# Optimization experiments

Hardware: AMD Instinct MI355X
Metric: run time of the kernel (lower is better)

Reference implementation:

```python
import jax, jax.numpy as jnp
import numpy as np

N_NODES = 50000
N_EDGES = 800000
IN_CH, HID_CH, OUT_CH = 256, 128, 64


def setup_inputs() -> dict:
    key = jax.random.key(0)
    k1, k2, k3, k4 = jax.random.split(key, 4)
    x = jax.random.normal(k1, (N_NODES, IN_CH), dtype=jnp.float32)
    edge_index = jax.random.randint(k2, (2, N_EDGES), 0, N_NODES, dtype=jnp.int64)
    # Glorot-style init for the GCN weight matrices, zero bias (PyG default)
    W1 = jax.random.normal(k3, (IN_CH, HID_CH), dtype=jnp.float32) * (1.0 / np.sqrt(IN_CH))
    b1 = jnp.zeros((HID_CH,), dtype=jnp.float32)
    W2 = jax.random.normal(k4, (HID_CH, OUT_CH), dtype=jnp.float32) * (1.0 / np.sqrt(HID_CH))
    b2 = jnp.zeros((OUT_CH,), dtype=jnp.float32)
    return {"x": x, "edge_index": edge_index, "W1": W1, "b1": b1, "W2": W2, "b2": b2}


def _gcn_conv(x, W, b, src, dst, dinv_sqrt, n_nodes):
    # linear transform then degree-normalized scatter-add aggregation
    h = x @ W                                        # [N, F_out]
    norm = dinv_sqrt[src] * dinv_sqrt[dst]           # [E+N]
    msg = h[src] * norm[:, None]                     # gather + scale
    out = jax.ops.segment_sum(msg, dst, num_segments=n_nodes)
    return out + b


def reference(x, edge_index, W1, b1, W2, b2):
    n_nodes = x.shape[0]
    loops = jnp.arange(n_nodes, dtype=edge_index.dtype)
    src = jnp.concatenate([edge_index[0], loops])    # add self-loops (PyG default)
    dst = jnp.concatenate([edge_index[1], loops])
    # symmetric normalization: deg computed over targets incl. self-loops
    deg = jax.ops.segment_sum(jnp.ones_like(dst, dtype=x.dtype), dst, num_segments=n_nodes)
    dinv_sqrt = jnp.where(deg > 0, jax.lax.rsqrt(deg), 0.0)
    h = jax.nn.relu(_gcn_conv(x, W1, b1, src, dst, dinv_sqrt, n_nodes))
    return _gcn_conv(h, W2, b2, src, dst, dinv_sqrt, n_nodes)
```

## Files before the change

### kernel.cpp

```cpp
#include <hip/hip_runtime.h>


typedef __attribute__((ext_vector_type(4))) float floatx4;
typedef _Float16 __attribute__((ext_vector_type(8))) half8v;

#define BUCK_SH 6
#define BUCK    64
#define NBLK    256

#define AS1(p) ((const __attribute__((address_space(1))) void*)(p))
#define AS3(p) ((__attribute__((address_space(3))) void*)(p))

__device__ __forceinline__ int edge_id(const int* __restrict__ ei, int is64, long long pos) {
    return is64 ? ei[2 * pos] : ei[(int)pos];
}

__device__ __forceinline__ int detect_is64(const int* __restrict__ ei) {
    __shared__ int nz;
    if (threadIdx.x == 0) nz = 0;
    __syncthreads();
    if (threadIdx.x < 256 && ei[2 * threadIdx.x + 1] != 0) atomicOr(&nz, 1);
    __syncthreads();
    return (nz == 0) ? 1 : 0;
}

__device__ __forceinline__ void convW_one(const float* W, _Float16* Wt, int K, int Nc, int idx) {
    if (idx >= K * Nc) return;
    int k = idx / Nc, n = idx % Nc;
    Wt[(long long)n * K + k] = (_Float16)W[idx];
}

__global__ void __launch_bounds__(256)
hist2convW_kernel(const int* __restrict__ ei, int* __restrict__ hist2,
                  int E, int NB, int chunk,
                  const float* __restrict__ W1, _Float16* __restrict__ W1t,
                  const float* __restrict__ W2, _Float16* __restrict__ W2t) {
    __shared__ int h[1024];
    const int t = threadIdx.x;
    const int is64 = detect_is64(ei);
    for (int i = t; i < NB; i += 256) h[i] = 0;
    __syncthreads();
    const int lo = blockIdx.x * chunk;
    const int hi = min(E, lo + chunk);
    for (int e = lo + t; e < hi; e += 256) {
        int d = edge_id(ei, is64, (long long)E + e);
        atomicAdd(&h[d >> BUCK_SH], 1);
    }
    __syncthreads();
    for (int i = t; i < NB; i += 256) hist2[(long long)blockIdx.x * NB + i] = h[i];
    {
        int gtid = blockIdx.x * 256 + t;
        convW_one(W1, W1t, 256, 128, gtid);
        int g2 = gtid - 256 * 128;
        if (g2 >= 0) convW_one(W2, W2t, 128, 64, g2);
    }
}

__global__ void __launch_bounds__(256)
wavescan_kernel(const int* __restrict__ hist2, int* __restrict__ start2t,
                int* __restrict__ colsum, int NB) {
    const int wid  = (blockIdx.x * 256 + threadIdx.x) >> 6;
    const int lane = threadIdx.x & 63;
    if (wid >= NB) return;
    int carry = 0;
    for (int c = 0; c < NBLK; c += 64) {
        int v = hist2[(long long)(c + lane) * NB + wid];
        int incl = v;
#pragma unroll
        for (int s = 1; s < 64; s <<= 1) {
            int u = __shfl_up(incl, s, 64);
            if (lane >= s) incl += u;
        }
        start2t[(long long)wid * NBLK + c + lane] = carry + incl - v;
        carry += __shfl(incl, 63, 64);
    }
    if (lane == 0) colsum[wid] = carry;
}

__global__ void __launch_bounds__(1024)
basescan_kernel(const int* __restrict__ colsum, int* __restrict__ bbase, int NB, int E) {
    __shared__ int sm[1024];
    const int t = threadIdx.x;
    int v = (t < NB) ? colsum[t] : 0;
    sm[t] = v;
    __syncthreads();
    for (int s = 1; s < 1024; s <<= 1) {
        int u = (t >= s) ? sm[t - s] : 0;
        __syncthreads();
        sm[t] += u;
        __syncthreads();
    }
    if (t < NB) bbase[t] = sm[t] - v;
    if (t == 0) bbase[NB] = E;
}

__global__ void __launch_bounds__(256)
scatter2_kernel(const int* __restrict__ ei, const int* __restrict__ bbase,
                const int* __restrict__ start2t, unsigned* __restrict__ ebuf,
                int E, int NB, int chunk) {
    __shared__ int hcur[1024];
    const int t = threadIdx.x;
    const int is64 = detect_is64(ei);
    for (int i = t; i < NB; i += 256)
        hcur[i] = bbase[i] + start2t[(long long)i * NBLK + blockIdx.x];
    __syncthreads();
    const int lo = blockIdx.x * chunk;
    const int hi = min(E, lo + chunk);
    for (int e = lo + t; e < hi; e += 256) {
        int s = edge_id(ei, is64, e);
        int d = edge_id(ei, is64, (long long)E + e);
        int pos = atomicAdd(&hcur[d >> BUCK_SH], 1);
        ebuf[pos] = (unsigned)s | ((unsigned)(d & (BUCK - 1)) << 26);
    }
}

__global__ void __launch_bounds__(256)
csrbuild_kernel(const unsigned* __restrict__ ebuf, const int* __restrict__ bbase,
                int* __restrict__ offs, float* __restrict__ dinv,
                int* __restrict__ csr, int N, int NB, int E) {
    __shared__ int cnt[BUCK], exc[BUCK], cur[BUCK];
    const int b = blockIdx.x;
    const int t = threadIdx.x;
    if (t < BUCK) { cnt[t] = 0; cur[t] = 0; }
    __syncthreads();
    const int lo = bbase[b], hi = bbase[b + 1];
    for (int i = lo + t; i < hi; i += blockDim.x)
        atomicAdd(&cnt[ebuf[i] >> 26], 1);
    __syncthreads();
    if (t == 0) {
        int run = 0;
        for (int l = 0; l < BUCK; ++l) { exc[l] = run; run += cnt[l]; }
    }
    __syncthreads();
    if (t < BUCK) {
        int n = b * BUCK + t;
        if (n < N) {
            offs[n] = lo + exc[t];
            dinv[n] = rsqrtf(1.0f + (float)cnt[t]);
        }
    }
    if (b == NB - 1 && t == 0) offs[N] = E;
    for (int i = lo + t; i < hi; i += blockDim.x) {
        unsigned e = ebuf[i];
        int l = e >> 26;
        int p = lo + exc[l] + atomicAdd(&cur[l], 1);
        csr[p] = (int)(e & 0x03FFFFFFu);
    }
}

template <int NCOL, int K>
__launch_bounds__(256)
__global__ void gemm_f16_kernel(const float* __restrict__ A,
                                const _Float16* __restrict__ Bt,
                                _Float16* __restrict__ C, int M) {
    constexpr int NCB = NCOL / 16;
    constexpr int BM = 128, BK = 64;
    constexpr int NC = K / BK;
    constexpr int UNITS = BM * BK / 4;
    __shared__ float As[2][BM * BK];

    const int tid  = threadIdx.x;
    const int wave = tid >> 6;
    const int lane = tid & 63;
    const int n15  = lane & 15;
    const int q    = lane >> 4;
    const int row0 = blockIdx.x * BM;

    floatx4 acc[2][NCB];
#pragma unroll
    for (int rt = 0; rt < 2; ++rt)
#pragma unroll
        for (int c = 0; c < NCB; ++c) acc[rt][c] = (floatx4){0.f, 0.f, 0.f, 0.f};

    auto stage = [&](int buf, int kc) {
#pragma unroll
        for (int j = 0; j < UNITS / 256; ++j) {
            int g = j * 256 + tid;
            int r = g >> 4;
            int u = (g & 15) ^ (r & 15);
            int gr = row0 + r;
            if (gr >= M) gr = M - 1;
            const float* gp = &A[(long long)gr * K + kc + u * 4];
            float* lp = &As[buf][g * 4];
            __builtin_amdgcn_global_load_lds(AS1(gp), AS3(lp), 16, 0, 0);
        }
    };

    stage(0, 0);
    __syncthreads();

#pragma unroll
    for (int c = 0; c < NC; ++c) {
        if (c + 1 < NC) stage((c + 1) & 1, (c + 1) * BK);
        const int buf = c & 1;
#pragma unroll
        for (int ks = 0; ks < 2; ++ks) {
            half8v af[2];
#pragma unroll
            for (int rt = 0; rt < 2; ++rt) {
                const int R = wave * 32 + rt * 16 + n15;
                const int u0 = ks * 8 + q * 2;
                const int p0 = (u0)     ^ (R & 15);
                const int p1 = (u0 + 1) ^ (R & 15);
                float4 f0 = *(const float4*)&As[buf][R * BK + p0 * 4];
                float4 f1 = *(const float4*)&As[buf][R * BK + p1 * 4];
                af[rt][0] = (_Float16)f0.x; af[rt][1] = (_Float16)f0.y;
                af[rt][2] = (_Float16)f0.z; af[rt][3] = (_Float16)f0.w;
                af[rt][4] = (_Float16)f1.x; af[rt][5] = (_Float16)f1.y;
                af[rt][6] = (_Float16)f1.z; af[rt][7] = (_Float16)f1.w;
            }
#pragma unroll
            for (int cb = 0; cb < NCB; ++cb) {
                const _Float16* bp = &Bt[(long long)(cb * 16 + n15) * K + c * BK + ks * 32 + q * 8];
                half8v bf = *(const half8v*)bp;
                acc[0][cb] = __builtin_amdgcn_mfma_f32_16x16x32_f16(af[0], bf, acc[0][cb], 0, 0, 0);
                acc[1][cb] = __builtin_amdgcn_mfma_f32_16x16x32_f16(af[1], bf, acc[1][cb], 0, 0, 0);
            }
        }
        if (c + 1 < NC) __syncthreads();
    }

#pragma unroll
    for (int rt = 0; rt < 2; ++rt) {
#pragma unroll
        for (int cb = 0; cb < NCB; ++cb) {
            int col = cb * 16 + n15;
#pragma unroll
            for (int r = 0; r < 4; ++r) {
                int gr = row0 + wave * 32 + rt * 16 + q * 4 + r;
                if (gr < M) C[(long long)gr * NCOL + col] = (_Float16)acc[rt][cb][r];
            }
        }
    }
}

__launch_bounds__(256)
__global__ void gatherg2_kernel(const _Float16* __restrict__ h,
                                const int* __restrict__ csr,
                                const int* __restrict__ offs,
                                const float* __restrict__ dinv,
                                const float* __restrict__ bias,
                                const _Float16* __restrict__ Bt,
                                _Float16* __restrict__ C,
                                int N) {
    constexpr int F = 128;
    constexpr int NCOL = 64;
    constexpr int L = F / 8;
    constexpr int NPB = 256 / L;
    constexpr int CAP = 1536;
    __shared__ _Float16 Ash[NPB * F];
    __shared__ float wL[CAP];

    const int r  = threadIdx.x / L;
    const int l  = threadIdx.x % L;
    const int c8 = l * 8;
    const int n  = blockIdx.x * NPB + r;

    const int n0   = blockIdx.x * NPB;
    const int nend = min(n0 + NPB, N);
    const int lo   = offs[n0];
    const int cntS = min(offs[nend] - lo, CAP);
    for (int i = threadIdx.x; i < cntS; i += 256)
        wL[i] = dinv[__builtin_nontemporal_load(&csr[lo + i])];
    __syncthreads();

    float acc[8];
    if (n < N) {
        const float di = dinv[n];
        half8v hs = *(const half8v*)&h[(long long)n * F + c8];
        const float sd = di * di;
#pragma unroll
        for (int j = 0; j < 8; ++j) acc[j] = (float)hs[j] * sd;

        const int end = offs[n + 1];
        for (int j = offs[n]; j < end; j += 8) {
            int s[8];
            float ws[8];
            half8v v[8];
#pragma unroll
            for (int u = 0; u < 8; ++u) {
                int jj = j + u;
                s[u] = __builtin_nontemporal_load(&csr[jj < end ? jj : end - 1]);
            }
#pragma unroll
            for (int u = 0; u < 8; ++u) {
                int jj = j + u;
                float w = (jj - lo < CAP) ? wL[jj - lo] : dinv[s[u]];
                ws[u] = (jj < end) ? w * di : 0.f;
            }
#pragma unroll
            for (int u = 0; u < 8; ++u) v[u] = *(const half8v*)&h[(long long)s[u] * F + c8];
#pragma unroll
            for (int u = 0; u < 8; ++u) {
#pragma unroll
                for (int t = 0; t < 8; ++t) acc[t] = fmaf((float)v[u][t], ws[u], acc[t]);
            }
        }
        float4 b0 = *(const float4*)&bias[c8];
        float4 b1v = *(const float4*)&bias[c8 + 4];
        float bb[8] = {b0.x, b0.y, b0.z, b0.w, b1v.x, b1v.y, b1v.z, b1v.w};
#pragma unroll
        for (int t = 0; t < 8; ++t) acc[t] = fmaxf(acc[t] + bb[t], 0.f);
    } else {
#pragma unroll
        for (int t = 0; t < 8; ++t) acc[t] = 0.f;
    }

    half8v hv;
#pragma unroll
    for (int t = 0; t < 8; ++t) hv[t] = (_Float16)acc[t];
    *(half8v*)&Ash[(r * 16 + (l ^ r)) * 8] = hv;
    __syncthreads();

    {
        const int lane = threadIdx.x & 63;
        const int wv   = threadIdx.x >> 6;
        const int n15  = lane & 15;
        const int q    = lane >> 4;
        floatx4 acc2 = (floatx4){0.f, 0.f, 0.f, 0.f};
#pragma unroll
        for (int kc = 0; kc < 4; ++kc) {
            const int u = (kc * 4 + q) ^ n15;
            half8v af = *(const half8v*)&Ash[(n15 * 16 + u) * 8];
            const _Float16* bp = &Bt[(long long)(wv * 16 + n15) * F + kc * 32 + q * 8];
            half8v bf = *(const half8v*)bp;
            acc2 = __builtin_amdgcn_mfma_f32_16x16x32_f16(af, bf, acc2, 0, 0, 0);
        }
        const int col = wv * 16 + n15;
#pragma unroll
        for (int rr = 0; rr < 4; ++rr) {
            int gr = blockIdx.x * NPB + q * 4 + rr;
            if (gr < N) C[(long long)gr * NCOL + col] = (_Float16)acc2[rr];
        }
    }
}

template <int F, int RELU>
__launch_bounds__(256)
__global__ void gatherh_kernel(const _Float16* __restrict__ h, const int* __restrict__ csr,
                               const int* __restrict__ offs, const float* __restrict__ dinv,
                               const float* __restrict__ bias, float* __restrict__ out, int N) {
    constexpr int L = F / 8;
    constexpr int NPB = 256 / L;
    constexpr int CAP = 2048;
    __shared__ float wL[CAP];
    const int n = blockIdx.x * NPB + threadIdx.x / L;
    const int c8 = (threadIdx.x % L) * 8;

    const int n0   = blockIdx.x * NPB;
    const int nend = min(n0 + NPB, N);
    const int lo   = offs[n0];
    const int cntS = min(offs[nend] - lo, CAP);
    for (int i = threadIdx.x; i < cntS; i += 256)
        wL[i] = dinv[__builtin_nontemporal_load(&csr[lo + i])];
    __syncthreads();

    if (n >= N) return;

    const float di = dinv[n];
    half8v hs = *(const half8v*)&h[(long long)n * F + c8];
    float acc[8];
    const float sd = di * di;
#pragma unroll
    for (int j = 0; j < 8; ++j) acc[j] = (float)hs[j] * sd;

    const int beg = offs[n], end = offs[n + 1];
    int s[8];
    if (beg < end) {
#pragma unroll
        for (int u = 0; u < 8; ++u) {
            int jj = beg + u;
            s[u] = __builtin_nontemporal_load(&csr[jj < end ? jj : end - 1]);
        }
    }
    for (int j = beg; j < end; j += 8) {
        int sn[8];
        const int jn = j + 8;
#pragma unroll
        for (int u = 0; u < 8; ++u) {
            int jj = jn + u;
            sn[u] = __builtin_nontemporal_load(&csr[jj < end ? jj : end - 1]);
        }
        float ws[8];
        half8v v[8];
#pragma unroll
        for (int u = 0; u < 8; ++u) {
            int jj = j + u;
            float w = (jj - lo < CAP) ? wL[jj - lo] : dinv[s[u]];
            ws[u] = (jj < end) ? w * di : 0.f;
        }
#pragma unroll
        for (int u = 0; u < 8; ++u) v[u] = *(const half8v*)&h[(long long)s[u] * F + c8];
#pragma unroll
        for (int u = 0; u < 8; ++u) {
#pragma unroll
            for (int t = 0; t < 8; ++t) acc[t] = fmaf((float)v[u][t], ws[u], acc[t]);
        }
#pragma unroll
        for (int u = 0; u < 8; ++u) s[u] = sn[u];
    }

    float4 b0 = *(const float4*)&bias[c8];
    float4 b1 = *(const float4*)&bias[c8 + 4];
    float bb[8] = {b0.x, b0.y, b0.z, b0.w, b1.x, b1.y, b1.z, b1.w};
#pragma unroll
    for (int t = 0; t < 8; ++t) {
        acc[t] += bb[t];
        if (RELU) acc[t] = fmaxf(acc[t], 0.f);
    }
    float* o = &out[(long long)n * F + c8];
    floatx4 o0 = (floatx4){acc[0], acc[1], acc[2], acc[3]};
    floatx4 o1 = (floatx4){acc[4], acc[5], acc[6], acc[7]};
    __builtin_nontemporal_store(o0, (floatx4*)o);
    __builtin_nontemporal_store(o1, (floatx4*)(o + 4));
}

extern "C" void kernel_launch(void* const* d_in, const int* in_sizes, int n_in,
                              void* d_out, int out_size, void* d_ws, size_t ws_size,
                              hipStream_t stream) {
    const float* x  = (const float*)d_in[0];
    const int*   ei = (const int*)d_in[1];
    const float* W1 = (const float*)d_in[2];
    const float* b1 = (const float*)d_in[3];
    const float* W2 = (const float*)d_in[4];
    const float* b2 = (const float*)d_in[5];
    float* out = (float*)d_out;

    const int IN_CH = 256, HID = 128, OUT = 64;
    const int N = in_sizes[0] / IN_CH;
    const int E = in_sizes[1] / 2;
    const int NB = (N + BUCK - 1) / BUCK;
    const int chunk = (E + NBLK - 1) / NBLK;

    char* w = (char*)d_ws;
    size_t off_b = 0;
    auto alloc = [&](size_t bytes) { void* p = w + off_b; off_b = (off_b + bytes + 255) & ~(size_t)255; return p; };
    int*   hist2   = (int*)alloc((size_t)NBLK * NB * 4);
    int*   start2t = (int*)alloc((size_t)NB * NBLK * 4);
    int*   colsum  = (int*)alloc((size_t)NB * 4);
    int*   bbase   = (int*)alloc((size_t)(NB + 1) * 4);
    int*   offs    = (int*)alloc((size_t)(N + 1) * 4);
    float* dinv    = (float*)alloc((size_t)N * 4);
    unsigned* ebuf = (unsigned*)alloc((size_t)E * 4);
    int*   csr     = (int*)alloc((size_t)E * 4);
    _Float16* W1t  = (_Float16*)alloc((size_t)IN_CH * HID * 2);
    _Float16* W2t  = (_Float16*)alloc((size_t)HID * OUT * 2);
    _Float16* h1   = (_Float16*)alloc((size_t)N * HID * 2);
    _Float16* h2   = (_Float16*)alloc((size_t)N * OUT * 2);

    hist2convW_kernel<<<NBLK, 256, 0, stream>>>(ei, hist2, E, NB, chunk,
                                                W1, W1t, W2, W2t);
    wavescan_kernel<<<(NB * 64 + 255) / 256, 256, 0, stream>>>(hist2, start2t, colsum, NB);
    basescan_kernel<<<1, 1024, 0, stream>>>(colsum, bbase, NB, E);
    scatter2_kernel<<<NBLK, 256, 0, stream>>>(ei, bbase, start2t, ebuf, E, NB, chunk);
    csrbuild_kernel<<<NB, 256, 0, stream>>>(ebuf, bbase, offs, dinv, csr, N, NB, E);

    gemm_f16_kernel<128, 256><<<(N + 127) / 128, 256, 0, stream>>>(x, W1t, h1, N);
    gatherg2_kernel<<<(N + 15) / 16, 256, 0, stream>>>(h1, csr, offs, dinv, b1, W2t, h2, N);
    gatherh_kernel<64, 0><<<(N * 8 + 255) / 256, 256, 0, stream>>>(h2, csr, offs, dinv, b2, out, N);
}
```

Before: 212.3 us.

## Fuse base scan into scatter and co-schedule CSR build with first GEMM

Folds the single-block base scan into every scatter block, which each recompute the bucket bases redundantly; block 0 writes them to global memory. The CSR build and the first GEMM become one launch that dispatches on block index, so the two independent stages overlap and two kernel launches are removed. Nontemporal loads and stores on csr and the output are also switched to ordinary accesses. In exchange, every csrbuild block now reserves the GEMM's 64KB shared memory, which limits its occupancy, and each scatter block repeats the scan.

```diff
diff --git a/kernel.cpp b/kernel.cpp
--- a/kernel.cpp
+++ b/kernel.cpp
@@ -77,33 +77,48 @@
     if (lane == 0) colsum[wid] = carry;
 }
 
-__global__ void __launch_bounds__(1024)
-basescan_kernel(const int* __restrict__ colsum, int* __restrict__ bbase, int NB, int E) {
-    __shared__ int sm[1024];
-    const int t = threadIdx.x;
-    int v = (t < NB) ? colsum[t] : 0;
-    sm[t] = v;
-    __syncthreads();
-    for (int s = 1; s < 1024; s <<= 1) {
-        int u = (t >= s) ? sm[t - s] : 0;
-        __syncthreads();
-        sm[t] += u;
-        __syncthreads();
-    }
-    if (t < NB) bbase[t] = sm[t] - v;
-    if (t == 0) bbase[NB] = E;
-}
-
 __global__ void __launch_bounds__(256)
-scatter2_kernel(const int* __restrict__ ei, const int* __restrict__ bbase,
-                const int* __restrict__ start2t, unsigned* __restrict__ ebuf,
-                int E, int NB, int chunk) {
+scatter2b_kernel(const int* __restrict__ ei, const int* __restrict__ colsum,
+                 const int* __restrict__ start2t, unsigned* __restrict__ ebuf,
+                 int* __restrict__ bbase_g, int E, int NB, int chunk) {
+    __shared__ int tsum[256];
+    __shared__ int bb[1024];
     __shared__ int hcur[1024];
     const int t = threadIdx.x;
     const int is64 = detect_is64(ei);
+
+    int c[4];
+#pragma unroll
+    for (int k = 0; k < 4; ++k) {
+        int i = t * 4 + k;
+        c[k] = (i < NB) ? colsum[i] : 0;
+    }
+    tsum[t] = c[0] + c[1] + c[2] + c[3];
+    __syncthreads();
+    int v = tsum[t];
+    for (int s = 1; s < 256; s <<= 1) {
+        int u = (t >= s) ? tsum[t - s] : 0;
+        __syncthreads();
+        tsum[t] += u;
+        __syncthreads();
+    }
+    int run = tsum[t] - v;
+#pragma unroll
+    for (int k = 0; k < 4; ++k) {
+        bb[t * 4 + k] = run;
+        run += c[k];
+    }
+    __syncthreads();
+
+    if (blockIdx.x == 0) {
+        for (int i = t; i < NB; i += 256) bbase_g[i] = bb[i];
+        if (t == 0) bbase_g[NB] = E;
+    }
+
     for (int i = t; i < NB; i += 256)
-        hcur[i] = bbase[i] + start2t[(long long)i * NBLK + blockIdx.x];
-    __syncthreads();
+        hcur[i] = bb[i] + start2t[(long long)i * NBLK + blockIdx.x];
+    __syncthreads();
+
     const int lo = blockIdx.x * chunk;
     const int hi = min(E, lo + chunk);
     for (int e = lo + t; e < hi; e += 256) {
@@ -114,57 +129,23 @@
     }
 }
 
-__global__ void __launch_bounds__(256)
-csrbuild_kernel(const unsigned* __restrict__ ebuf, const int* __restrict__ bbase,
-                int* __restrict__ offs, float* __restrict__ dinv,
-                int* __restrict__ csr, int N, int NB, int E) {
-    __shared__ int cnt[BUCK], exc[BUCK], cur[BUCK];
-    const int b = blockIdx.x;
-    const int t = threadIdx.x;
-    if (t < BUCK) { cnt[t] = 0; cur[t] = 0; }
-    __syncthreads();
-    const int lo = bbase[b], hi = bbase[b + 1];
-    for (int i = lo + t; i < hi; i += blockDim.x)
-        atomicAdd(&cnt[ebuf[i] >> 26], 1);
-    __syncthreads();
-    if (t == 0) {
-        int run = 0;
-        for (int l = 0; l < BUCK; ++l) { exc[l] = run; run += cnt[l]; }
-    }
-    __syncthreads();
-    if (t < BUCK) {
-        int n = b * BUCK + t;
-        if (n < N) {
-            offs[n] = lo + exc[t];
-            dinv[n] = rsqrtf(1.0f + (float)cnt[t]);
-        }
-    }
-    if (b == NB - 1 && t == 0) offs[N] = E;
-    for (int i = lo + t; i < hi; i += blockDim.x) {
-        unsigned e = ebuf[i];
-        int l = e >> 26;
-        int p = lo + exc[l] + atomicAdd(&cur[l], 1);
-        csr[p] = (int)(e & 0x03FFFFFFu);
-    }
-}
-
-template <int NCOL, int K>
-__launch_bounds__(256)
-__global__ void gemm_f16_kernel(const float* __restrict__ A,
-                                const _Float16* __restrict__ Bt,
-                                _Float16* __restrict__ C, int M) {
+__device__ __forceinline__ void gemm1_body(char* smem,
+                                           const float* __restrict__ A,
+                                           const _Float16* __restrict__ Bt,
+                                           _Float16* __restrict__ C, int M, int bid) {
+    constexpr int NCOL = 128, K = 256;
     constexpr int NCB = NCOL / 16;
     constexpr int BM = 128, BK = 64;
     constexpr int NC = K / BK;
     constexpr int UNITS = BM * BK / 4;
-    __shared__ float As[2][BM * BK];
+    float* As = (float*)smem;
 
     const int tid  = threadIdx.x;
     const int wave = tid >> 6;
     const int lane = tid & 63;
     const int n15  = lane & 15;
     const int q    = lane >> 4;
-    const int row0 = blockIdx.x * BM;
+    const int row0 = bid * BM;
 
     floatx4 acc[2][NCB];
 #pragma unroll
@@ -181,7 +162,7 @@
             int gr = row0 + r;
             if (gr >= M) gr = M - 1;
             const float* gp = &A[(long long)gr * K + kc + u * 4];
-            float* lp = &As[buf][g * 4];
+            float* lp = &As[buf * (BM * BK) + g * 4];
             __builtin_amdgcn_global_load_lds(AS1(gp), AS3(lp), 16, 0, 0);
         }
     };
@@ -202,8 +183,8 @@
                 const int u0 = ks * 8 + q * 2;
                 const int p0 = (u0)     ^ (R & 15);
                 const int p1 = (u0 + 1) ^ (R & 15);
-                float4 f0 = *(const float4*)&As[buf][R * BK + p0 * 4];
-                float4 f1 = *(const float4*)&As[buf][R * BK + p1 * 4];
+                float4 f0 = *(const float4*)&As[buf * (BM * BK) + R * BK + p0 * 4];
+                float4 f1 = *(const float4*)&As[buf * (BM * BK) + R * BK + p1 * 4];
                 af[rt][0] = (_Float16)f0.x; af[rt][1] = (_Float16)f0.y;
                 af[rt][2] = (_Float16)f0.z; af[rt][3] = (_Float16)f0.w;
                 af[rt][4] = (_Float16)f1.x; af[rt][5] = (_Float16)f1.y;
@@ -231,6 +212,57 @@
                 if (gr < M) C[(long long)gr * NCOL + col] = (_Float16)acc[rt][cb][r];
             }
         }
+    }
+}
+
+__device__ __forceinline__ void csrbuild_body(char* smem,
+                                              const unsigned* __restrict__ ebuf,
+                                              const int* __restrict__ bbase,
+                                              int* __restrict__ offs, float* __restrict__ dinv,
+                                              int* __restrict__ csr, int N, int NB, int E, int b) {
+    int* cnt = (int*)smem;
+    int* exc = cnt + BUCK;
+    int* cur = exc + BUCK;
+    const int t = threadIdx.x;
+    if (t < BUCK) { cnt[t] = 0; cur[t] = 0; }
+    __syncthreads();
+    const int lo = bbase[b], hi = bbase[b + 1];
+    for (int i = lo + t; i < hi; i += 256)
+        atomicAdd(&cnt[ebuf[i] >> 26], 1);
+    __syncthreads();
+    if (t == 0) {
+        int run = 0;
+        for (int l = 0; l < BUCK; ++l) { exc[l] = run; run += cnt[l]; }
+    }
+    __syncthreads();
+    if (t < BUCK) {
+        int n = b * BUCK + t;
+        if (n < N) {
+            offs[n] = lo + exc[t];
+            dinv[n] = rsqrtf(1.0f + (float)cnt[t]);
+        }
+    }
+    if (b == NB - 1 && t == 0) offs[N] = E;
+    for (int i = lo + t; i < hi; i += 256) {
+        unsigned e = ebuf[i];
+        int l = e >> 26;
+        int p = lo + exc[l] + atomicAdd(&cur[l], 1);
+        csr[p] = (int)(e & 0x03FFFFFFu);
+    }
+}
+
+__global__ void __launch_bounds__(256)
+csrgemm_kernel(const unsigned* __restrict__ ebuf, const int* __restrict__ bbase,
+               int* __restrict__ offs, float* __restrict__ dinv, int* __restrict__ csr,
+               int N, int NB, int E,
+               const float* __restrict__ A, const _Float16* __restrict__ Bt,
+               _Float16* __restrict__ C, int M, int nGemm) {
+    __shared__ __align__(16) char smem[65536];
+    const int bid = blockIdx.x;
+    if (bid < nGemm) {
+        gemm1_body(smem, A, Bt, C, M, bid);
+    } else {
+        csrbuild_body(smem, ebuf, bbase, offs, dinv, csr, N, NB, E, bid - nGemm);
     }
 }
 
@@ -261,7 +293,7 @@
     const int lo   = offs[n0];
     const int cntS = min(offs[nend] - lo, CAP);
     for (int i = threadIdx.x; i < cntS; i += 256)
-        wL[i] = dinv[__builtin_nontemporal_load(&csr[lo + i])];
+        wL[i] = dinv[csr[lo + i]];
     __syncthreads();
 
     float acc[8];
@@ -280,7 +312,7 @@
 #pragma unroll
             for (int u = 0; u < 8; ++u) {
                 int jj = j + u;
-                s[u] = __builtin_nontemporal_load(&csr[jj < end ? jj : end - 1]);
+                s[u] = csr[jj < end ? jj : end - 1];
             }
 #pragma unroll
             for (int u = 0; u < 8; ++u) {
@@ -352,7 +384,7 @@
     const int lo   = offs[n0];
     const int cntS = min(offs[nend] - lo, CAP);
     for (int i = threadIdx.x; i < cntS; i += 256)
-        wL[i] = dinv[__builtin_nontemporal_load(&csr[lo + i])];
+        wL[i] = dinv[csr[lo + i]];
     __syncthreads();
 
     if (n >= N) return;
@@ -370,7 +402,7 @@
 #pragma unroll
         for (int u = 0; u < 8; ++u) {
             int jj = beg + u;
-            s[u] = __builtin_nontemporal_load(&csr[jj < end ? jj : end - 1]);
+            s[u] = csr[jj < end ? jj : end - 1];
         }
     }
     for (int j = beg; j < end; j += 8) {
@@ -379,7 +411,7 @@
 #pragma unroll
         for (int u = 0; u < 8; ++u) {
             int jj = jn + u;
-            sn[u] = __builtin_nontemporal_load(&csr[jj < end ? jj : end - 1]);
+            sn[u] = csr[jj < end ? jj : end - 1];
         }
         float ws[8];
         half8v v[8];
@@ -409,10 +441,8 @@
         if (RELU) acc[t] = fmaxf(acc[t], 0.f);
     }
     float* o = &out[(long long)n * F + c8];
-    floatx4 o0 = (floatx4){acc[0], acc[1], acc[2], acc[3]};
-    floatx4 o1 = (floatx4){acc[4], acc[5], acc[6], acc[7]};
-    __builtin_nontemporal_store(o0, (floatx4*)o);
-    __builtin_nontemporal_store(o1, (floatx4*)(o + 4));
+    *(float4*)o       = make_float4(acc[0], acc[1], acc[2], acc[3]);
+    *(float4*)(o + 4) = make_float4(acc[4], acc[5], acc[6], acc[7]);
 }
 
 extern "C" void kernel_launch(void* const* d_in, const int* in_sizes, int n_in,
@@ -431,6 +461,7 @@
     const int E = in_sizes[1] / 2;
     const int NB = (N + BUCK - 1) / BUCK;
     const int chunk = (E + NBLK - 1) / NBLK;
+    const int nGemm = (N + 127) / 128;
 
     char* w = (char*)d_ws;
     size_t off_b = 0;
@@ -451,11 +482,9 @@
     hist2convW_kernel<<<NBLK, 256, 0, stream>>>(ei, hist2, E, NB, chunk,
                                                 W1, W1t, W2, W2t);
     wavescan_kernel<<<(NB * 64 + 255) / 256, 256, 0, stream>>>(hist2, start2t, colsum, NB);
-    basescan_kernel<<<1, 1024, 0, stream>>>(colsum, bbase, NB, E);
-    scatter2_kernel<<<NBLK, 256, 0, stream>>>(ei, bbase, start2t, ebuf, E, NB, chunk);
-    csrbuild_kernel<<<NB, 256, 0, stream>>>(ebuf, bbase, offs, dinv, csr, N, NB, E);
-
-    gemm_f16_kernel<128, 256><<<(N + 127) / 128, 256, 0, stream>>>(x, W1t, h1, N);
+    scatter2b_kernel<<<NBLK, 256, 0, stream>>>(ei, colsum, start2t, ebuf, bbase, E, NB, chunk);
+    csrgemm_kernel<<<nGemm + NB, 256, 0, stream>>>(ebuf, bbase, offs, dinv, csr,
+                                                   N, NB, E, x, W1t, h1, N, nGemm);
     gatherg2_kernel<<<(N + 15) / 16, 256, 0, stream>>>(h1, csr, offs, dinv, b1, W2t, h2, N);
     gatherh_kernel<64, 0><<<(N * 8 + 255) / 256, 256, 0, stream>>>(h2, csr, offs, dinv, b2, out, N);
 }
```

Measured after the change: 194.8 us, median of 2. 1.09x faster.
